# Kernel optimization log

Hardware: AMD Instinct MI355X
Metric: run time of the kernel (lower is better)

Reference implementation:

```python
import jax, jax.numpy as jnp
import numpy as np

EDGE_LABELS = jnp.arange(5, dtype=jnp.float32)  # possible ratings 0..4
NUM_USERS, NUM_MOVIES, HIDDEN, NUM_EDGES = 100000, 50000, 64, 1000000


def setup_inputs() -> dict:
    key = jax.random.key(0)
    k1, k2, k3, k4 = jax.random.split(key, 4)
    z_user = jax.random.normal(k1, (NUM_USERS, HIDDEN), dtype=jnp.float32)
    z_movie = jax.random.normal(k2, (NUM_MOVIES, HIDDEN), dtype=jnp.float32)
    rel_emb = jax.random.normal(k3, (EDGE_LABELS.shape[0], HIDDEN), dtype=jnp.float32)
    edge_label_index = jax.random.randint(k4, (2, NUM_EDGES), 0, NUM_MOVIES, dtype=jnp.int64)
    return {"z_user": z_user, "z_movie": z_movie, "rel_emb": rel_emb,
            "edge_label_index": edge_label_index}


def reference(z_user, z_movie, rel_emb, edge_label_index):
    # Gather endpoint embeddings once: [E, H]
    z_src = z_user[edge_label_index[0]]
    z_dst = z_movie[edge_label_index[1]]
    # Per-relation bilinear score: sum_h z_src*rel_r*z_dst -> [E, R]
    scores = jnp.einsum('eh,rh->er', z_src * z_dst, rel_emb)
    probs = jax.nn.softmax(scores, axis=1)
    # Expected rating under softmax distribution: [E]
    predicted_ratings = probs @ EDGE_LABELS
    return predicted_ratings
```

## Files before the change

### kernel.cpp

```cpp
#include <hip/hip_runtime.h>
#include <hip/hip_fp16.h>

#define H 64
#define R 5

typedef float    v2f __attribute__((ext_vector_type(2)));
typedef _Float16 v2h __attribute__((ext_vector_type(2)));

static __device__ __forceinline__ v2f fma2(v2f a, v2f b, v2f c) {
#if __has_builtin(__builtin_elementwise_fma)
    return __builtin_elementwise_fma(a, b, c);
#else
    return a * b + c;
#endif
}

static __device__ __forceinline__ float dot2(v2h a, v2h b, float c) {
#if __has_builtin(__builtin_amdgcn_fdot2)
    return __builtin_amdgcn_fdot2(a, b, c, false);
#else
    return (float)a.x * (float)b.x + (float)a.y * (float)b.y + c;
#endif
}

static __device__ __forceinline__ v2h bch(unsigned u) {
    return __builtin_bit_cast(v2h, u);
}

static __device__ __forceinline__ unsigned h2pair(float a, float b) {
    __half2 h = __floats2half2_rn(a, b);
    return *(const unsigned*)&h;
}

__global__ __launch_bounds__(256) void convert_f16_kernel(
    const float4* __restrict__ zu4, const float4* __restrict__ zm4,
    const float4* __restrict__ rel4,
    uint4* __restrict__ wu, uint4* __restrict__ wm, uint4* __restrict__ wr,
    int n_u_chunks, int n_m_chunks, int n_r_chunks)
{
    int t = blockIdx.x * blockDim.x + threadIdx.x;
    const float4* src;
    uint4* dst;
    int c;
    if (t < n_u_chunks)                   { src = zu4;  dst = wu; c = t; }
    else if (t < n_u_chunks + n_m_chunks) { src = zm4;  dst = wm; c = t - n_u_chunks; }
    else if (t < n_u_chunks + n_m_chunks + n_r_chunks)
                                          { src = rel4; dst = wr; c = t - n_u_chunks - n_m_chunks; }
    else return;
    float4 f0 = src[2 * c];
    float4 f1 = src[2 * c + 1];
    uint4 o;
    o.x = h2pair(f0.x, f0.y);
    o.y = h2pair(f0.z, f0.w);
    o.z = h2pair(f1.x, f1.y);
    o.w = h2pair(f1.z, f1.w);
    dst[c] = o;
}

__global__ __launch_bounds__(256) void edge_decoder_f16s_kernel(
    const uint4* __restrict__ wu,
    const uint4* __restrict__ wm,
    const uint4* __restrict__ wr,
    const int*   __restrict__ idx,
    float*       __restrict__ out,
    int E)
{
    int tid  = blockIdx.x * blockDim.x + threadIdx.x;
    int l    = tid & 3;
    int base = tid & ~3;
    if (base >= E) return;

    int su_l = 0, sm_l = 0;
    if (tid < E) { su_l = idx[tid]; sm_l = idx[E + tid]; }

    int su0 = __shfl(su_l, 0, 4);
    int su1 = __shfl(su_l, 1, 4);
    int su2 = __shfl(su_l, 2, 4);
    int su3 = __shfl(su_l, 3, 4);
    int sm0 = __shfl(sm_l, 0, 4);
    int sm1 = __shfl(sm_l, 1, 4);
    int sm2 = __shfl(sm_l, 2, 4);
    int sm3 = __shfl(sm_l, 3, 4);

#define ROWS(j)                                          \
    uint4 a0_##j = wu[(size_t)su##j * 8 + l];            \
    uint4 a1_##j = wu[(size_t)su##j * 8 + 4 + l];        \
    uint4 b0_##j = wm[(size_t)sm##j * 8 + l];            \
    uint4 b1_##j = wm[(size_t)sm##j * 8 + 4 + l];
    ROWS(0) ROWS(1) ROWS(2) ROWS(3)
#undef ROWS

#define RELS(r)                                          \
    uint4 w0_##r = wr[r * 8 + l];                        \
    uint4 w1_##r = wr[r * 8 + 4 + l];
    RELS(0) RELS(1) RELS(2) RELS(3) RELS(4)
#undef RELS

#define MAKE_P(j)                                        \
    v2h p##j##_0 = bch(a0_##j.x) * bch(b0_##j.x);        \
    v2h p##j##_1 = bch(a0_##j.y) * bch(b0_##j.y);        \
    v2h p##j##_2 = bch(a0_##j.z) * bch(b0_##j.z);        \
    v2h p##j##_3 = bch(a0_##j.w) * bch(b0_##j.w);        \
    v2h p##j##_4 = bch(a1_##j.x) * bch(b1_##j.x);        \
    v2h p##j##_5 = bch(a1_##j.y) * bch(b1_##j.y);        \
    v2h p##j##_6 = bch(a1_##j.z) * bch(b1_##j.z);        \
    v2h p##j##_7 = bch(a1_##j.w) * bch(b1_##j.w);
    MAKE_P(0) MAKE_P(1) MAKE_P(2) MAKE_P(3)
#undef MAKE_P

    bool c1 = (l & 1) != 0;
    bool c2 = (l & 2) != 0;

#define SCORE(j, r)                                                   \
    dot2(p##j##_7, bch(w1_##r.w), dot2(p##j##_6, bch(w1_##r.z),       \
    dot2(p##j##_5, bch(w1_##r.y), dot2(p##j##_4, bch(w1_##r.x),       \
    dot2(p##j##_3, bch(w0_##r.w), dot2(p##j##_2, bch(w0_##r.z),       \
    dot2(p##j##_1, bch(w0_##r.y), dot2(p##j##_0, bch(w0_##r.x), 0.f))))))))

    float sc0, sc1, sc2, sc3, sc4;
#define REDUCE(r, scr) {                                              \
        float s0 = SCORE(0, r);                                       \
        float s1 = SCORE(1, r);                                       \
        float s2 = SCORE(2, r);                                       \
        float s3 = SCORE(3, r);                                       \
        s0 += __shfl_xor(s0, 1); s1 += __shfl_xor(s1, 1);             \
        s2 += __shfl_xor(s2, 1); s3 += __shfl_xor(s3, 1);             \
        s0 += __shfl_xor(s0, 2); s1 += __shfl_xor(s1, 2);             \
        s2 += __shfl_xor(s2, 2); s3 += __shfl_xor(s3, 2);             \
        scr = c2 ? (c1 ? s3 : s2) : (c1 ? s1 : s0);                   \
    }
    REDUCE(0, sc0) REDUCE(1, sc1) REDUCE(2, sc2) REDUCE(3, sc3) REDUCE(4, sc4)
#undef REDUCE
#undef SCORE

    float mx = fmaxf(fmaxf(fmaxf(sc0, sc1), fmaxf(sc2, sc3)), sc4);
    float e0 = __expf(sc0 - mx);
    float e1 = __expf(sc1 - mx);
    float e2 = __expf(sc2 - mx);
    float e3 = __expf(sc3 - mx);
    float e4 = __expf(sc4 - mx);
    float den = e0 + e1 + e2 + e3 + e4;
    float num = fmaf(4.f, e4, fmaf(3.f, e3, fmaf(2.f, e2, e1)));
    if (tid < E) out[tid] = num * __frcp_rn(den);
}

__global__ __launch_bounds__(256) void edge_decoder_f32_kernel(
    const float4* __restrict__ zu4, const float4* __restrict__ zm4,
    const float4* __restrict__ rel4, const int* __restrict__ idx,
    float* __restrict__ out, int E)
{
    int tid = blockIdx.x * blockDim.x + threadIdx.x;
    int l   = threadIdx.x & 3;
    int e   = tid >> 2;
    if (e >= E) return;
    int su = idx[e];
    int sm = idx[E + e];
    const float4* arow = zu4 + su * 16;
    const float4* brow = zm4 + sm * 16;
    v2f plo[4], phi[4];
#pragma unroll
    for (int i = 0; i < 4; ++i) {
        float4 av = arow[4 * i + l];
        float4 bv = brow[4 * i + l];
        v2f alo = {av.x, av.y}, ahi = {av.z, av.w};
        v2f blo = {bv.x, bv.y}, bhi = {bv.z, bv.w};
        plo[i] = alo * blo;
        phi[i] = ahi * bhi;
    }
    float s[R];
#pragma unroll
    for (int r = 0; r < R; ++r) {
        v2f acc = {0.f, 0.f};
#pragma unroll
        for (int i = 0; i < 4; ++i) {
            float4 w = rel4[r * 16 + 4 * i + l];
            acc = fma2(plo[i], (v2f){w.x, w.y}, acc);
            acc = fma2(phi[i], (v2f){w.z, w.w}, acc);
        }
        s[r] = acc.x + acc.y;
    }
#pragma unroll
    for (int r = 0; r < R; ++r) s[r] += __shfl_xor(s[r], 1);
#pragma unroll
    for (int r = 0; r < R; ++r) s[r] += __shfl_xor(s[r], 2);
    if (l == 0) {
        float mx = fmaxf(fmaxf(fmaxf(s[0], s[1]), fmaxf(s[2], s[3])), s[4]);
        float e0 = __expf(s[0] - mx);
        float e1 = __expf(s[1] - mx);
        float e2 = __expf(s[2] - mx);
        float e3 = __expf(s[3] - mx);
        float e4 = __expf(s[4] - mx);
        float den = e0 + e1 + e2 + e3 + e4;
        float num = fmaf(4.f, e4, fmaf(3.f, e3, fmaf(2.f, e2, e1)));
        out[e] = num * __frcp_rn(den);
    }
}

extern "C" void kernel_launch(void* const* d_in, const int* in_sizes, int n_in,
                              void* d_out, int out_size, void* d_ws, size_t ws_size,
                              hipStream_t stream) {
    const float4* zu4  = (const float4*)d_in[0];
    const float4* zm4  = (const float4*)d_in[1];
    const float4* rel4 = (const float4*)d_in[2];
    const int*    idx  = (const int*)d_in[3];
    float* out = (float*)d_out;

    int E  = in_sizes[3] / 2;
    int nu = in_sizes[0] / H;
    int nm = in_sizes[1] / H;

    size_t need = (size_t)(nu + nm + R) * H * 2;
    int block = 256;

    if (ws_size >= need) {
        uint4* wu = (uint4*)d_ws;
        uint4* wm = wu + (size_t)nu * 8;
        uint4* wr = wm + (size_t)nm * 8;

        int n_u_chunks = nu * (H / 8);
        int n_m_chunks = nm * (H / 8);
        int n_r_chunks = R * (H / 8);
        int conv_threads = n_u_chunks + n_m_chunks + n_r_chunks;
        int conv_grid = (conv_threads + block - 1) / block;
        convert_f16_kernel<<<conv_grid, block, 0, stream>>>(
            zu4, zm4, rel4, wu, wm, wr, n_u_chunks, n_m_chunks, n_r_chunks);

        long long threads = (long long)E;
        int grid = (int)((threads + block - 1) / block);
        edge_decoder_f16s_kernel<<<grid, block, 0, stream>>>(
            wu, wm, wr, idx, out, E);
    } else {
        long long threads = (long long)E * 4;
        int grid = (int)((threads + block - 1) / block);
        edge_decoder_f32_kernel<<<grid, block, 0, stream>>>(
            zu4, zm4, rel4, idx, out, E);
    }
}
```

Baseline: 115.5 us.

## Spread each edge row across 8 lanes with butterfly transpose-reduction

Changes the f16 edge kernel from 4-lane groups to 8-lane groups. Each lane now loads one 16-byte chunk per row for 8 edges, so a row's 128 bytes are fetched by 8 lanes together. The cross-lane reduction becomes a select-and-exchange butterfly that needs 7 shuffles per relation instead of 8, and each lane ends with one edge's score. This makes gathers more coalesced per row and cuts per-lane loads, in exchange for more index shuffles and wider select logic.

```diff
diff --git a/kernel.cpp b/kernel.cpp
--- a/kernel.cpp
+++ b/kernel.cpp
@@ -57,7 +57,7 @@
     dst[c] = o;
 }
 
-__global__ __launch_bounds__(256) void edge_decoder_f16s_kernel(
+__global__ __launch_bounds__(256) void edge_decoder_f16o_kernel(
     const uint4* __restrict__ wu,
     const uint4* __restrict__ wm,
     const uint4* __restrict__ wr,
@@ -66,68 +66,76 @@
     int E)
 {
     int tid  = blockIdx.x * blockDim.x + threadIdx.x;
-    int l    = tid & 3;
-    int base = tid & ~3;
+    int l    = tid & 7;
+    int base = tid & ~7;
     if (base >= E) return;
 
     int su_l = 0, sm_l = 0;
     if (tid < E) { su_l = idx[tid]; sm_l = idx[E + tid]; }
 
-    int su0 = __shfl(su_l, 0, 4);
-    int su1 = __shfl(su_l, 1, 4);
-    int su2 = __shfl(su_l, 2, 4);
-    int su3 = __shfl(su_l, 3, 4);
-    int sm0 = __shfl(sm_l, 0, 4);
-    int sm1 = __shfl(sm_l, 1, 4);
-    int sm2 = __shfl(sm_l, 2, 4);
-    int sm3 = __shfl(sm_l, 3, 4);
+    int su0 = __shfl(su_l, 0, 8);
+    int su1 = __shfl(su_l, 1, 8);
+    int su2 = __shfl(su_l, 2, 8);
+    int su3 = __shfl(su_l, 3, 8);
+    int su4 = __shfl(su_l, 4, 8);
+    int su5 = __shfl(su_l, 5, 8);
+    int su6 = __shfl(su_l, 6, 8);
+    int su7 = __shfl(su_l, 7, 8);
+    int sm0 = __shfl(sm_l, 0, 8);
+    int sm1 = __shfl(sm_l, 1, 8);
+    int sm2 = __shfl(sm_l, 2, 8);
+    int sm3 = __shfl(sm_l, 3, 8);
+    int sm4 = __shfl(sm_l, 4, 8);
+    int sm5 = __shfl(sm_l, 5, 8);
+    int sm6 = __shfl(sm_l, 6, 8);
+    int sm7 = __shfl(sm_l, 7, 8);
 
 #define ROWS(j)                                          \
-    uint4 a0_##j = wu[(size_t)su##j * 8 + l];            \
-    uint4 a1_##j = wu[(size_t)su##j * 8 + 4 + l];        \
-    uint4 b0_##j = wm[(size_t)sm##j * 8 + l];            \
-    uint4 b1_##j = wm[(size_t)sm##j * 8 + 4 + l];
-    ROWS(0) ROWS(1) ROWS(2) ROWS(3)
+    uint4 a_##j = wu[(size_t)su##j * 8 + l];             \
+    uint4 b_##j = wm[(size_t)sm##j * 8 + l];
+    ROWS(0) ROWS(1) ROWS(2) ROWS(3) ROWS(4) ROWS(5) ROWS(6) ROWS(7)
 #undef ROWS
 
 #define RELS(r)                                          \
-    uint4 w0_##r = wr[r * 8 + l];                        \
-    uint4 w1_##r = wr[r * 8 + 4 + l];
+    uint4 w_##r = wr[r * 8 + l];
     RELS(0) RELS(1) RELS(2) RELS(3) RELS(4)
 #undef RELS
 
 #define MAKE_P(j)                                        \
-    v2h p##j##_0 = bch(a0_##j.x) * bch(b0_##j.x);        \
-    v2h p##j##_1 = bch(a0_##j.y) * bch(b0_##j.y);        \
-    v2h p##j##_2 = bch(a0_##j.z) * bch(b0_##j.z);        \
-    v2h p##j##_3 = bch(a0_##j.w) * bch(b0_##j.w);        \
-    v2h p##j##_4 = bch(a1_##j.x) * bch(b1_##j.x);        \
-    v2h p##j##_5 = bch(a1_##j.y) * bch(b1_##j.y);        \
-    v2h p##j##_6 = bch(a1_##j.z) * bch(b1_##j.z);        \
-    v2h p##j##_7 = bch(a1_##j.w) * bch(b1_##j.w);
+    v2h p##j##_0 = bch(a_##j.x) * bch(b_##j.x);          \
+    v2h p##j##_1 = bch(a_##j.y) * bch(b_##j.y);          \
+    v2h p##j##_2 = bch(a_##j.z) * bch(b_##j.z);          \
+    v2h p##j##_3 = bch(a_##j.w) * bch(b_##j.w);
     MAKE_P(0) MAKE_P(1) MAKE_P(2) MAKE_P(3)
+    MAKE_P(4) MAKE_P(5) MAKE_P(6) MAKE_P(7)
 #undef MAKE_P
 
     bool c1 = (l & 1) != 0;
     bool c2 = (l & 2) != 0;
+    bool c4 = (l & 4) != 0;
 
 #define SCORE(j, r)                                                   \
-    dot2(p##j##_7, bch(w1_##r.w), dot2(p##j##_6, bch(w1_##r.z),       \
-    dot2(p##j##_5, bch(w1_##r.y), dot2(p##j##_4, bch(w1_##r.x),       \
-    dot2(p##j##_3, bch(w0_##r.w), dot2(p##j##_2, bch(w0_##r.z),       \
-    dot2(p##j##_1, bch(w0_##r.y), dot2(p##j##_0, bch(w0_##r.x), 0.f))))))))
+    dot2(p##j##_3, bch(w_##r.w), dot2(p##j##_2, bch(w_##r.z),         \
+    dot2(p##j##_1, bch(w_##r.y), dot2(p##j##_0, bch(w_##r.x), 0.f))))
 
     float sc0, sc1, sc2, sc3, sc4;
-#define REDUCE(r, scr) {                                              \
-        float s0 = SCORE(0, r);                                       \
-        float s1 = SCORE(1, r);                                       \
-        float s2 = SCORE(2, r);                                       \
-        float s3 = SCORE(3, r);                                       \
-        s0 += __shfl_xor(s0, 1); s1 += __shfl_xor(s1, 1);             \
-        s2 += __shfl_xor(s2, 1); s3 += __shfl_xor(s3, 1);             \
-        s0 += __shfl_xor(s0, 2); s1 += __shfl_xor(s1, 2);             \
-        s2 += __shfl_xor(s2, 2); s3 += __shfl_xor(s3, 2);             \
-        scr = c2 ? (c1 ? s3 : s2) : (c1 ? s1 : s0);                   \
+#define REDUCE(r, scr) {                                                   \
+        float s0 = SCORE(0, r); float s1 = SCORE(1, r);                    \
+        float s2 = SCORE(2, r); float s3 = SCORE(3, r);                    \
+        float s4 = SCORE(4, r); float s5 = SCORE(5, r);                    \
+        float s6 = SCORE(6, r); float s7 = SCORE(7, r);                    \
+        float m01 = c1 ? s1 : s0, o01 = c1 ? s0 : s1;                      \
+        float m23 = c1 ? s3 : s2, o23 = c1 ? s2 : s3;                      \
+        float m45 = c1 ? s5 : s4, o45 = c1 ? s4 : s5;                      \
+        float m67 = c1 ? s7 : s6, o67 = c1 ? s6 : s7;                      \
+        m01 += __shfl_xor(o01, 1); m23 += __shfl_xor(o23, 1);              \
+        m45 += __shfl_xor(o45, 1); m67 += __shfl_xor(o67, 1);              \
+        float n03 = c2 ? m23 : m01, q03 = c2 ? m01 : m23;                  \
+        float n47 = c2 ? m67 : m45, q47 = c2 ? m45 : m67;                  \
+        n03 += __shfl_xor(q03, 2); n47 += __shfl_xor(q47, 2);              \
+        float fv  = c4 ? n47 : n03, qf  = c4 ? n03 : n47;                  \
+        fv += __shfl_xor(qf, 4);                                           \
+        scr = fv;                                                          \
     }
     REDUCE(0, sc0) REDUCE(1, sc1) REDUCE(2, sc2) REDUCE(3, sc3) REDUCE(4, sc4)
 #undef REDUCE
@@ -227,7 +235,7 @@
 
         long long threads = (long long)E;
         int grid = (int)((threads + block - 1) / block);
-        edge_decoder_f16s_kernel<<<grid, block, 0, stream>>>(
+        edge_decoder_f16o_kernel<<<grid, block, 0, stream>>>(
             wu, wm, wr, idx, out, E);
     } else {
         long long threads = (long long)E * 4;
```

After: 115.2 us. Within noise of the previous version (-0.3%).
